# Kernel tuning notes

Hardware: AMD Instinct MI355X
Metric: run time of the kernel (lower is better)

Reference implementation:

```python
import jax, jax.numpy as jnp
import numpy as np

EPS = 1e-8

def _mlp(z, W1, b1, W2, b2):
    # Two Blocks (Linear + ReLU), widths per n_layers=[512,128]
    z = jax.nn.relu(z @ W1 + b1)
    z = jax.nn.relu(z @ W2 + b2)
    return z

def setup_inputs() -> dict:
    key = jax.random.key(0)
    ks = jax.random.split(key, 5)
    B, N, D = 1024, 30000, 256
    H1, H2 = 512, 128
    x = jax.random.normal(ks[0], (B, D), dtype=jnp.float32)
    sub_x = jax.random.normal(ks[1], (N, D), dtype=jnp.float32)
    sub_y = jax.random.uniform(ks[2], (N,), dtype=jnp.float32)
    W1 = jax.random.normal(ks[3], (D, H1), dtype=jnp.float32) * (1.0 / np.sqrt(D))
    b1 = jnp.zeros((H1,), dtype=jnp.float32)
    W2 = jax.random.normal(ks[4], (H1, H2), dtype=jnp.float32) * (1.0 / np.sqrt(H1))
    b2 = jnp.zeros((H2,), dtype=jnp.float32)
    return {"x": x, "sub_x": sub_x, "sub_y": sub_y, "W1": W1, "b1": b1, "W2": W2, "b2": b2}

def reference(x, sub_x, sub_y, W1, b1, W2, b2):
    h = _mlp(x, W1, b1, W2, b2)          # [B, d]
    sh = _mlp(sub_x, W1, b1, W2, b2)     # [N, d]
    # Pairwise squared euclidean via ||a||^2 + ||b||^2 - 2 a.b (GEMM form,
    # same math as the broadcasted diff-and-reduce in the torch code)
    x2 = jnp.sum(h * h, axis=-1, keepdims=True)        # [B, 1]
    s2 = jnp.sum(sh * sh, axis=-1)[None, :]            # [1, N]
    d2 = jnp.maximum(x2 + s2 - 2.0 * (h @ sh.T), 0.0)  # [B, N]
    dist = jnp.sqrt(d2 + EPS)
    alpha = jax.nn.softmax(-dist, axis=-1)             # [B, N]
    return alpha @ sub_y                               # [B]
```

## Files before the change

kernel.cpp:

```cpp
#include <hip/hip_runtime.h>
#include <hip/hip_bf16.h>
#include <math.h>

#define EPSF 1e-8f

typedef __attribute__((ext_vector_type(8))) short bf16x8;
typedef __attribute__((ext_vector_type(4))) float f32x4;

static __device__ __forceinline__ unsigned short f2bf(float f) {
    __hip_bfloat16 h = __float2bfloat16(f);
    return *reinterpret_cast<unsigned short*>(&h);
}
static __device__ __forceinline__ float bf2f(unsigned short u) {
    __hip_bfloat16 h;
    *reinterpret_cast<unsigned short*>(&h) = u;
    return __bfloat162float(h);
}

static __device__ __forceinline__ void async16(void* lds, const void* g) {
    __builtin_amdgcn_global_load_lds(
        (const __attribute__((address_space(1))) unsigned int*)g,
        (__attribute__((address_space(3))) unsigned int*)lds, 16, 0, 0);
}

__global__ __launch_bounds__(256) void split_combined(
    const float* __restrict__ subx, const float* __restrict__ x,
    unsigned short* __restrict__ H, unsigned short* __restrict__ L,
    float* __restrict__ gl, float* __restrict__ gy, float* __restrict__ nrm,
    int n4, int nsubrow, int nrm4)
{
    int i = blockIdx.x * 256 + threadIdx.x;
    float4 z = make_float4(0.f, 0.f, 0.f, 0.f);
    if (i < 512) {
        if (i < 256) ((float4*)gl)[i] = z;
        else         ((float4*)gy)[i - 256] = z;
    }
    if (i < nrm4) ((float4*)nrm)[i] = z;
    if (i >= n4) return;
    int row = i >> 6;
    float4 v = (row < nsubrow)
        ? ((const float4*)subx)[i]
        : ((const float4*)x)[i - (size_t)nsubrow * 64];
    unsigned short h0 = f2bf(v.x), h1 = f2bf(v.y), h2 = f2bf(v.z), h3 = f2bf(v.w);
    unsigned short l0 = f2bf(v.x - bf2f(h0));
    unsigned short l1 = f2bf(v.y - bf2f(h1));
    unsigned short l2 = f2bf(v.z - bf2f(h2));
    unsigned short l3 = f2bf(v.w - bf2f(h3));
    uint2 hp, lp;
    hp.x = ((unsigned)h1 << 16) | h0;  hp.y = ((unsigned)h3 << 16) | h2;
    lp.x = ((unsigned)l1 << 16) | l0;  lp.y = ((unsigned)l3 << 16) | l2;
    ((uint2*)H)[i] = hp;
    ((uint2*)L)[i] = lp;
}

__global__ __launch_bounds__(256) void tsplit(
    const float* __restrict__ W, unsigned short* __restrict__ HT,
    unsigned short* __restrict__ LT, int kshift, int N, int total)
{
    int idx = blockIdx.x * 256 + threadIdx.x;
    if (idx >= total) return;
    int K = 1 << kshift;
    int n = idx >> kshift, k = idx & (K - 1);
    float w = W[(size_t)k * N + n];
    unsigned short h = f2bf(w);
    HT[idx] = h;
    LT[idx] = f2bf(w - bf2f(h));
}

__global__ __launch_bounds__(256, 5) void gemm_l1(
    const unsigned short* __restrict__ Ah, const unsigned short* __restrict__ Al,
    const unsigned short* __restrict__ BhT, const unsigned short* __restrict__ BlT,
    const float* __restrict__ bias, unsigned short* __restrict__ Cout, int M)
{
    const int K = 256, N = 512;
    __shared__ __align__(16) unsigned short smem[4608];
    unsigned short* sBh = smem;
    unsigned short* sBl = smem + 2048;

    const int nb = gridDim.x;
    const int per = nb >> 3, rem = nb & 7;
    const int xcd = blockIdx.x & 7, slot = blockIdx.x >> 3;
    const int newbid = xcd * per + min(xcd, rem) + slot;
    const int m0 = (newbid >> 3) * 128, n0 = (newbid & 7) * 64;

    const int t = threadIdx.x, wave = t >> 6, lane = t & 63;
    const int quad = lane >> 4, lq = lane & 15;
    const int rsub = lane >> 2, kc8 = (lane & 3) * 8;

    const unsigned short* gb[2];
    unsigned short* lb[2];
    #pragma unroll
    for (int q = 0; q < 2; ++q) {
        int c = wave * 2 + q;
        int plane = c >> 2, rc = c & 3;
        gb[q] = (plane ? BlT : BhT) + (size_t)(n0 + rc * 16 + rsub) * K + kc8;
        lb[q] = (plane ? sBl : sBh) + rc * 512;
    }
    const unsigned short* pAh[2];
    const unsigned short* pAl[2];
    #pragma unroll
    for (int mi = 0; mi < 2; ++mi) {
        size_t r = (size_t)min(m0 + wave * 32 + mi * 16 + lq, M - 1) * K + quad * 8;
        pAh[mi] = Ah + r;
        pAl[mi] = Al + r;
    }

    f32x4 acc[2][4];
    #pragma unroll
    for (int i = 0; i < 2; ++i)
        #pragma unroll
        for (int j = 0; j < 4; ++j) acc[i][j] = (f32x4){0.f, 0.f, 0.f, 0.f};

    #pragma unroll
    for (int kc = 0; kc < 8; ++kc) {
        const int k0 = kc * 32;
        __syncthreads();
        #pragma unroll
        for (int q = 0; q < 2; ++q) async16(lb[q], gb[q] + k0);
        bf16x8 fAh[2], fAl[2];
        #pragma unroll
        for (int mi = 0; mi < 2; ++mi) {
            fAh[mi] = *(const bf16x8*)(pAh[mi] + k0);
            fAl[mi] = *(const bf16x8*)(pAl[mi] + k0);
        }
        __syncthreads();

        #pragma unroll
        for (int ni = 0; ni < 4; ++ni) {
            int off = ni * 512 + lq * 32 + quad * 8;
            bf16x8 fBh = *(const bf16x8*)&sBh[off];
            bf16x8 fBl = *(const bf16x8*)&sBl[off];
            #pragma unroll
            for (int mi = 0; mi < 2; ++mi) {
                f32x4 a = acc[mi][ni];
                a = __builtin_amdgcn_mfma_f32_16x16x32_bf16(fAh[mi], fBh, a, 0, 0, 0);
                a = __builtin_amdgcn_mfma_f32_16x16x32_bf16(fAh[mi], fBl, a, 0, 0, 0);
                a = __builtin_amdgcn_mfma_f32_16x16x32_bf16(fAl[mi], fBh, a, 0, 0, 0);
                acc[mi][ni] = a;
            }
        }
    }

    unsigned short* ctile = smem;
    float bv[4];
    #pragma unroll
    for (int ni = 0; ni < 4; ++ni) bv[ni] = bias[n0 + ni * 16 + lq];
    #pragma unroll
    for (int p = 0; p < 2; ++p) {
        __syncthreads();
        if ((wave >> 1) == p) {
            int lrow0 = (wave & 1) * 32;
            #pragma unroll
            for (int mi = 0; mi < 2; ++mi)
                #pragma unroll
                for (int ni = 0; ni < 4; ++ni)
                    #pragma unroll
                    for (int r = 0; r < 4; ++r) {
                        float v = fmaxf(acc[mi][ni][r] + bv[ni], 0.f);
                        ctile[(lrow0 + mi * 16 + quad * 4 + r) * 72 + ni * 16 + lq] = f2bf(v);
                    }
        }
        __syncthreads();
        #pragma unroll
        for (int it = 0; it < 2; ++it) {
            int flat = it * 256 + t;
            int row = flat >> 3, seg = flat & 7;
            int gm = m0 + p * 64 + row;
            if (gm < M) {
                bf16x8 v = *(const bf16x8*)&ctile[row * 72 + seg * 8];
                *(bf16x8*)&Cout[(size_t)gm * N + n0 + seg * 8] = v;
            }
        }
    }
}

__global__ __launch_bounds__(256, 5) void gemm_l2_norm(
    const unsigned short* __restrict__ A,
    const unsigned short* __restrict__ BhT, const unsigned short* __restrict__ BlT,
    const float* __restrict__ bias, unsigned short* __restrict__ Cout,
    float* __restrict__ nrm, int M)
{
    const int K = 512, N = 128;
    __shared__ __align__(16) unsigned short smem[4608];
    unsigned short* sBh = smem;
    unsigned short* sBl = smem + 2048;

    const int t = threadIdx.x, wave = t >> 6, lane = t & 63;
    const int quad = lane >> 4, lq = lane & 15;
    const int m0 = (blockIdx.x >> 1) * 128, n0 = (blockIdx.x & 1) * 64;
    const int rsub = lane >> 2, kc8 = (lane & 3) * 8;

    const unsigned short* gb[2];
    unsigned short* lb[2];
    #pragma unroll
    for (int q = 0; q < 2; ++q) {
        int c = wave * 2 + q;
        int plane = c >> 2, rc = c & 3;
        gb[q] = (plane ? BlT : BhT) + (size_t)(n0 + rc * 16 + rsub) * K + kc8;
        lb[q] = (plane ? sBl : sBh) + rc * 512;
    }
    const unsigned short* pA[2];
    #pragma unroll
    for (int mi = 0; mi < 2; ++mi)
        pA[mi] = A + (size_t)min(m0 + wave * 32 + mi * 16 + lq, M - 1) * K + quad * 8;

    f32x4 acc[2][4];
    #pragma unroll
    for (int i = 0; i < 2; ++i)
        #pragma unroll
        for (int j = 0; j < 4; ++j) acc[i][j] = (f32x4){0.f, 0.f, 0.f, 0.f};

    #pragma unroll
    for (int kc = 0; kc < 16; ++kc) {
        const int k0 = kc * 32;
        __syncthreads();
        #pragma unroll
        for (int q = 0; q < 2; ++q) async16(lb[q], gb[q] + k0);
        bf16x8 fA[2];
        #pragma unroll
        for (int mi = 0; mi < 2; ++mi) fA[mi] = *(const bf16x8*)(pA[mi] + k0);
        __syncthreads();

        #pragma unroll
        for (int ni = 0; ni < 4; ++ni) {
            int off = ni * 512 + lq * 32 + quad * 8;
            bf16x8 fBh = *(const bf16x8*)&sBh[off];
            bf16x8 fBl = *(const bf16x8*)&sBl[off];
            #pragma unroll
            for (int mi = 0; mi < 2; ++mi) {
                f32x4 a = acc[mi][ni];
                a = __builtin_amdgcn_mfma_f32_16x16x32_bf16(fA[mi], fBh, a, 0, 0, 0);
                a = __builtin_amdgcn_mfma_f32_16x16x32_bf16(fA[mi], fBl, a, 0, 0, 0);
                acc[mi][ni] = a;
            }
        }
    }

    unsigned short* ctile = smem;
    float bv[4];
    #pragma unroll
    for (int ni = 0; ni < 4; ++ni) bv[ni] = bias[n0 + ni * 16 + lq];
    #pragma unroll
    for (int p = 0; p < 2; ++p) {
        __syncthreads();
        if ((wave >> 1) == p) {
            int lrow0 = (wave & 1) * 32;
            #pragma unroll
            for (int mi = 0; mi < 2; ++mi)
                #pragma unroll
                for (int ni = 0; ni < 4; ++ni)
                    #pragma unroll
                    for (int r = 0; r < 4; ++r) {
                        float v = fmaxf(acc[mi][ni][r] + bv[ni], 0.f);
                        ctile[(lrow0 + mi * 16 + quad * 4 + r) * 72 + ni * 16 + lq] = f2bf(v);
                    }
        }
        __syncthreads();
        #pragma unroll
        for (int it = 0; it < 2; ++it) {
            int flat = it * 256 + t;
            int row = flat >> 3, seg = flat & 7;
            int gm = m0 + p * 64 + row;
            if (gm < M) {
                bf16x8 v = *(const bf16x8*)&ctile[row * 72 + seg * 8];
                *(bf16x8*)&Cout[(size_t)gm * N + n0 + seg * 8] = v;
                float s = 0.f;
                #pragma unroll
                for (int e = 0; e < 8; ++e) {
                    float f = bf2f((unsigned short)v[e]);
                    s = fmaf(f, f, s);
                }
                s += __shfl_down(s, 4, 8);
                s += __shfl_down(s, 2, 8);
                s += __shfl_down(s, 1, 8);
                if (seg == 0) atomicAdd(&nrm[gm], s);
            }
        }
    }
}

__global__ __launch_bounds__(256) void nca_flash_mfma(
    const unsigned short* __restrict__ emb, const float* __restrict__ nrm,
    const float* __restrict__ y, float* __restrict__ gl, float* __restrict__ gy,
    int N, int jspan)
{
    __shared__ __align__(16) unsigned short hA[8192];
    __shared__ __align__(16) unsigned short sB[16384];
    __shared__ float h2s[64], s2s[128], ys[128];

    const int t = threadIdx.x, wave = t >> 6, lane = t & 63;
    const int quad = lane >> 4, lq = lane & 15;
    const int rsub = lane >> 2, kc8 = (lane & 3) * 8;
    const int i0 = blockIdx.x * 64;
    const int j0base = blockIdx.y * jspan;
    const int jend = min(j0base + jspan, N);
    const unsigned short* hb = emb + (size_t)N * 128;

    #pragma unroll
    for (int q = 0; q < 4; ++q)
        async16(hA + (wave * 4 + q) * 512,
                hb + (size_t)(i0 + wave * 16 + rsub) * 128 + q * 32 + kc8);
    if (t < 64) h2s[t] = nrm[N + i0 + t];
    __syncthreads();

    float myh2[4];
    #pragma unroll
    for (int r = 0; r < 4; ++r) myh2[r] = h2s[wave * 16 + quad * 4 + r];

    float lacc[4] = {0.f, 0.f, 0.f, 0.f};
    float yacc[4] = {0.f, 0.f, 0.f, 0.f};

    for (int j0 = j0base; j0 < jend; j0 += 128) {
        __syncthreads();
        #pragma unroll
        for (int q = 0; q < 8; ++q) {
            int c = wave * 8 + q;
            int rc = c >> 2, kcq = c & 3;
            int jr = min(j0 + rc * 16 + rsub, jend - 1);
            async16(sB + c * 512, emb + (size_t)jr * 128 + kcq * 32 + kc8);
        }
        if (t < 128) {
            int j = j0 + t;
            s2s[t] = (j < jend) ? nrm[j] : 1e30f;
            ys[t]  = (j < jend) ? y[j] : 0.f;
        }
        __syncthreads();

        f32x4 acc[8];
        #pragma unroll
        for (int jt = 0; jt < 8; ++jt) acc[jt] = (f32x4){0.f, 0.f, 0.f, 0.f};
        #pragma unroll
        for (int kk = 0; kk < 4; ++kk) {
            bf16x8 a = *(const bf16x8*)&hA[(wave * 4 + kk) * 512 + lq * 32 + quad * 8];
            #pragma unroll
            for (int jt = 0; jt < 8; ++jt) {
                bf16x8 b = *(const bf16x8*)&sB[(jt * 4 + kk) * 512 + lq * 32 + quad * 8];
                acc[jt] = __builtin_amdgcn_mfma_f32_16x16x32_bf16(a, b, acc[jt], 0, 0, 0);
            }
        }

        #pragma unroll
        for (int jt = 0; jt < 8; ++jt) {
            int col = jt * 16 + lq;
            float ss = s2s[col];
            float sy = ys[col];
            #pragma unroll
            for (int r = 0; r < 4; ++r) {
                float d2 = myh2[r] + ss - 2.f * acc[jt][r];
                float d  = sqrtf(fmaxf(d2, 0.f) + EPSF);
                float p  = __expf(-d);
                lacc[r] += p;
                yacc[r]  = fmaf(p, sy, yacc[r]);
            }
        }
    }

    #pragma unroll
    for (int r = 0; r < 4; ++r) {
        #pragma unroll
        for (int off = 8; off > 0; off >>= 1) {
            lacc[r] += __shfl_down(lacc[r], off, 16);
            yacc[r] += __shfl_down(yacc[r], off, 16);
        }
    }
    if (lq == 0) {
        int rowl = wave * 16 + quad * 4;
        #pragma unroll
        for (int r = 0; r < 4; ++r) {
            atomicAdd(&gl[i0 + rowl + r], lacc[r]);
            atomicAdd(&gy[i0 + rowl + r], yacc[r]);
        }
    }
}

__global__ __launch_bounds__(256) void finalize_div(
    const float* __restrict__ gl, const float* __restrict__ gy,
    float* __restrict__ out, int B)
{
    int i = blockIdx.x * 256 + threadIdx.x;
    if (i < B) out[i] = gy[i] / gl[i];
}

extern "C" void kernel_launch(void* const* d_in, const int* in_sizes, int n_in,
                              void* d_out, int out_size, void* d_ws, size_t ws_size,
                              hipStream_t stream)
{
    const float* x    = (const float*)d_in[0];
    const float* subx = (const float*)d_in[1];
    const float* suby = (const float*)d_in[2];
    const float* W1   = (const float*)d_in[3];
    const float* b1   = (const float*)d_in[4];
    const float* W2   = (const float*)d_in[5];
    const float* b2   = (const float*)d_in[6];
    float* out = (float*)d_out;

    const int B = 1024, N = 30000, D = 256, H1 = 512, H2 = 128;
    const int M = N + B;

    char* wsb = (char*)d_ws;
    size_t off = 0;
    auto alloc = [&](size_t bytes) -> char* {
        char* p = wsb + off;
        off += (bytes + 255) & ~(size_t)255;
        return p;
    };
    unsigned short* cxh  = (unsigned short*)alloc((size_t)M * D * 2);
    unsigned short* cxl  = (unsigned short*)alloc((size_t)M * D * 2);
    unsigned short* w1hT = (unsigned short*)alloc((size_t)H1 * D * 2);
    unsigned short* w1lT = (unsigned short*)alloc((size_t)H1 * D * 2);
    unsigned short* w2hT = (unsigned short*)alloc((size_t)H2 * H1 * 2);
    unsigned short* w2lT = (unsigned short*)alloc((size_t)H2 * H1 * 2);
    unsigned short* z1   = (unsigned short*)alloc((size_t)M * H1 * 2);
    unsigned short* emb  = (unsigned short*)alloc((size_t)M * H2 * 2);
    float* nrm = (float*)alloc((size_t)M * 4);
    float* gl  = (float*)alloc((size_t)B * 4);
    float* gy  = (float*)alloc((size_t)B * 4);
    (void)ws_size; (void)in_sizes; (void)n_in; (void)out_size;

    dim3 blk(256);
    split_combined<<<dim3(M * D / 4 / 256), blk, 0, stream>>>(
        subx, x, cxh, cxl, gl, gy, nrm, M * D / 4, N, (M + 3) / 4);
    tsplit<<<dim3(D * H1 / 256), blk, 0, stream>>>(W1, w1hT, w1lT, 8, H1, D * H1);
    tsplit<<<dim3(H1 * H2 / 256), blk, 0, stream>>>(W2, w2hT, w2lT, 9, H2, H1 * H2);
    gemm_l1<<<dim3(((M + 127) / 128) * (H1 / 64)), blk, 0, stream>>>(
        cxh, cxl, w1hT, w1lT, b1, z1, M);
    gemm_l2_norm<<<dim3(((M + 127) / 128) * (H2 / 64)), blk, 0, stream>>>(
        z1, w2hT, w2lT, b2, emb, nrm, M);
    const int JSPAN = 512;
    const int NSPLIT = (N + JSPAN - 1) / JSPAN;
    nca_flash_mfma<<<dim3(B / 64, NSPLIT), blk, 0, stream>>>(
        emb, nrm, suby, gl, gy, N, JSPAN);
    finalize_div<<<dim3(B / 256), blk, 0, stream>>>(gl, gy, out, B);
}
```

Baseline: 184.4 us.

## Stage full B panels in LDS once and read flash operands directly from global

Both MLP GEMMs now load the entire hi/lo weight panel for the block into a 64KB LDS buffer with a single barrier, instead of staging one K-chunk per iteration between two barriers. gemm_l2_norm narrows its N tile to 32, doubles the grid and adds XCD-aware block remapping. The distance/softmax kernel drops LDS staging entirely and reads A fragments, B fragments, norms and labels straight from global memory with no barriers. The large LDS footprint cuts occupancy (launch bounds lowered to 2 blocks), and the global-direct flash loads depend on cache hit rates.

```diff
diff --git a/kernel.cpp b/kernel.cpp
--- a/kernel.cpp
+++ b/kernel.cpp
@@ -67,15 +67,13 @@
     LT[idx] = f2bf(w - bf2f(h));
 }
 
-__global__ __launch_bounds__(256, 5) void gemm_l1(
+__global__ __launch_bounds__(256, 2) void gemm_l1(
     const unsigned short* __restrict__ Ah, const unsigned short* __restrict__ Al,
     const unsigned short* __restrict__ BhT, const unsigned short* __restrict__ BlT,
     const float* __restrict__ bias, unsigned short* __restrict__ Cout, int M)
 {
     const int K = 256, N = 512;
-    __shared__ __align__(16) unsigned short smem[4608];
-    unsigned short* sBh = smem;
-    unsigned short* sBl = smem + 2048;
+    __shared__ __align__(16) unsigned short sB[32768];
 
     const int nb = gridDim.x;
     const int per = nb >> 3, rem = nb & 7;
@@ -87,15 +85,15 @@
     const int quad = lane >> 4, lq = lane & 15;
     const int rsub = lane >> 2, kc8 = (lane & 3) * 8;
 
-    const unsigned short* gb[2];
-    unsigned short* lb[2];
-    #pragma unroll
-    for (int q = 0; q < 2; ++q) {
-        int c = wave * 2 + q;
-        int plane = c >> 2, rc = c & 3;
-        gb[q] = (plane ? BlT : BhT) + (size_t)(n0 + rc * 16 + rsub) * K + kc8;
-        lb[q] = (plane ? sBl : sBh) + rc * 512;
-    }
+    #pragma unroll
+    for (int q = 0; q < 16; ++q) {
+        int c = wave * 16 + q;
+        int plane = c >> 5, idx = c & 31, nc = idx >> 3, kc = idx & 7;
+        const unsigned short* src = (plane ? BlT : BhT)
+            + (size_t)(n0 + nc * 16 + rsub) * K + kc * 32 + kc8;
+        async16(sB + c * 512, src);
+    }
+
     const unsigned short* pAh[2];
     const unsigned short* pAl[2];
     #pragma unroll
@@ -111,25 +109,22 @@
         #pragma unroll
         for (int j = 0; j < 4; ++j) acc[i][j] = (f32x4){0.f, 0.f, 0.f, 0.f};
 
+    __syncthreads();
+
     #pragma unroll
     for (int kc = 0; kc < 8; ++kc) {
         const int k0 = kc * 32;
-        __syncthreads();
-        #pragma unroll
-        for (int q = 0; q < 2; ++q) async16(lb[q], gb[q] + k0);
         bf16x8 fAh[2], fAl[2];
         #pragma unroll
         for (int mi = 0; mi < 2; ++mi) {
             fAh[mi] = *(const bf16x8*)(pAh[mi] + k0);
             fAl[mi] = *(const bf16x8*)(pAl[mi] + k0);
         }
-        __syncthreads();
-
         #pragma unroll
         for (int ni = 0; ni < 4; ++ni) {
-            int off = ni * 512 + lq * 32 + quad * 8;
-            bf16x8 fBh = *(const bf16x8*)&sBh[off];
-            bf16x8 fBl = *(const bf16x8*)&sBl[off];
+            int off = (ni * 8 + kc) * 512 + lq * 32 + quad * 8;
+            bf16x8 fBh = *(const bf16x8*)&sB[off];
+            bf16x8 fBl = *(const bf16x8*)&sB[16384 + off];
             #pragma unroll
             for (int mi = 0; mi < 2; ++mi) {
                 f32x4 a = acc[mi][ni];
@@ -141,7 +136,7 @@
         }
     }
 
-    unsigned short* ctile = smem;
+    unsigned short* ctile = sB;
     float bv[4];
     #pragma unroll
     for (int ni = 0; ni < 4; ++ni) bv[ni] = bias[n0 + ni * 16 + lq];
@@ -174,58 +169,58 @@
     }
 }
 
-__global__ __launch_bounds__(256, 5) void gemm_l2_norm(
+__global__ __launch_bounds__(256, 2) void gemm_l2_norm(
     const unsigned short* __restrict__ A,
     const unsigned short* __restrict__ BhT, const unsigned short* __restrict__ BlT,
     const float* __restrict__ bias, unsigned short* __restrict__ Cout,
     float* __restrict__ nrm, int M)
 {
     const int K = 512, N = 128;
-    __shared__ __align__(16) unsigned short smem[4608];
-    unsigned short* sBh = smem;
-    unsigned short* sBl = smem + 2048;
+    __shared__ __align__(16) unsigned short sB[32768];
+
+    const int nb = gridDim.x;
+    const int per = nb >> 3, rem = nb & 7;
+    const int xcd = blockIdx.x & 7, slot = blockIdx.x >> 3;
+    const int newbid = xcd * per + min(xcd, rem) + slot;
+    const int m0 = (newbid >> 2) * 128, n0 = (newbid & 3) * 32;
 
     const int t = threadIdx.x, wave = t >> 6, lane = t & 63;
     const int quad = lane >> 4, lq = lane & 15;
-    const int m0 = (blockIdx.x >> 1) * 128, n0 = (blockIdx.x & 1) * 64;
     const int rsub = lane >> 2, kc8 = (lane & 3) * 8;
 
-    const unsigned short* gb[2];
-    unsigned short* lb[2];
-    #pragma unroll
-    for (int q = 0; q < 2; ++q) {
-        int c = wave * 2 + q;
-        int plane = c >> 2, rc = c & 3;
-        gb[q] = (plane ? BlT : BhT) + (size_t)(n0 + rc * 16 + rsub) * K + kc8;
-        lb[q] = (plane ? sBl : sBh) + rc * 512;
-    }
+    #pragma unroll
+    for (int q = 0; q < 16; ++q) {
+        int c = wave * 16 + q;
+        int plane = c >> 5, idx = c & 31, nc = idx >> 4, kc = idx & 15;
+        const unsigned short* src = (plane ? BlT : BhT)
+            + (size_t)(n0 + nc * 16 + rsub) * K + kc * 32 + kc8;
+        async16(sB + c * 512, src);
+    }
+
     const unsigned short* pA[2];
     #pragma unroll
     for (int mi = 0; mi < 2; ++mi)
         pA[mi] = A + (size_t)min(m0 + wave * 32 + mi * 16 + lq, M - 1) * K + quad * 8;
 
-    f32x4 acc[2][4];
+    f32x4 acc[2][2];
     #pragma unroll
     for (int i = 0; i < 2; ++i)
         #pragma unroll
-        for (int j = 0; j < 4; ++j) acc[i][j] = (f32x4){0.f, 0.f, 0.f, 0.f};
+        for (int j = 0; j < 2; ++j) acc[i][j] = (f32x4){0.f, 0.f, 0.f, 0.f};
+
+    __syncthreads();
 
     #pragma unroll
     for (int kc = 0; kc < 16; ++kc) {
         const int k0 = kc * 32;
-        __syncthreads();
-        #pragma unroll
-        for (int q = 0; q < 2; ++q) async16(lb[q], gb[q] + k0);
         bf16x8 fA[2];
         #pragma unroll
         for (int mi = 0; mi < 2; ++mi) fA[mi] = *(const bf16x8*)(pA[mi] + k0);
-        __syncthreads();
-
-        #pragma unroll
-        for (int ni = 0; ni < 4; ++ni) {
-            int off = ni * 512 + lq * 32 + quad * 8;
-            bf16x8 fBh = *(const bf16x8*)&sBh[off];
-            bf16x8 fBl = *(const bf16x8*)&sBl[off];
+        #pragma unroll
+        for (int ni = 0; ni < 2; ++ni) {
+            int off = (ni * 16 + kc) * 512 + lq * 32 + quad * 8;
+            bf16x8 fBh = *(const bf16x8*)&sB[off];
+            bf16x8 fBl = *(const bf16x8*)&sB[16384 + off];
             #pragma unroll
             for (int mi = 0; mi < 2; ++mi) {
                 f32x4 a = acc[mi][ni];
@@ -236,114 +231,92 @@
         }
     }
 
-    unsigned short* ctile = smem;
-    float bv[4];
-    #pragma unroll
-    for (int ni = 0; ni < 4; ++ni) bv[ni] = bias[n0 + ni * 16 + lq];
-    #pragma unroll
-    for (int p = 0; p < 2; ++p) {
-        __syncthreads();
-        if ((wave >> 1) == p) {
-            int lrow0 = (wave & 1) * 32;
-            #pragma unroll
-            for (int mi = 0; mi < 2; ++mi)
-                #pragma unroll
-                for (int ni = 0; ni < 4; ++ni)
-                    #pragma unroll
-                    for (int r = 0; r < 4; ++r) {
-                        float v = fmaxf(acc[mi][ni][r] + bv[ni], 0.f);
-                        ctile[(lrow0 + mi * 16 + quad * 4 + r) * 72 + ni * 16 + lq] = f2bf(v);
-                    }
-        }
-        __syncthreads();
-        #pragma unroll
-        for (int it = 0; it < 2; ++it) {
-            int flat = it * 256 + t;
-            int row = flat >> 3, seg = flat & 7;
-            int gm = m0 + p * 64 + row;
-            if (gm < M) {
-                bf16x8 v = *(const bf16x8*)&ctile[row * 72 + seg * 8];
-                *(bf16x8*)&Cout[(size_t)gm * N + n0 + seg * 8] = v;
-                float s = 0.f;
-                #pragma unroll
-                for (int e = 0; e < 8; ++e) {
-                    float f = bf2f((unsigned short)v[e]);
-                    s = fmaf(f, f, s);
-                }
-                s += __shfl_down(s, 4, 8);
-                s += __shfl_down(s, 2, 8);
-                s += __shfl_down(s, 1, 8);
-                if (seg == 0) atomicAdd(&nrm[gm], s);
-            }
-        }
-    }
-}
-
-__global__ __launch_bounds__(256) void nca_flash_mfma(
+    __syncthreads();
+    unsigned short* ctile = sB;
+    float bv[2];
+    #pragma unroll
+    for (int ni = 0; ni < 2; ++ni) bv[ni] = bias[n0 + ni * 16 + lq];
+    #pragma unroll
+    for (int mi = 0; mi < 2; ++mi)
+        #pragma unroll
+        for (int ni = 0; ni < 2; ++ni)
+            #pragma unroll
+            for (int r = 0; r < 4; ++r) {
+                float v = fmaxf(acc[mi][ni][r] + bv[ni], 0.f);
+                ctile[(wave * 32 + mi * 16 + quad * 4 + r) * 36 + ni * 16 + lq] = f2bf(v);
+            }
+    __syncthreads();
+
+    #pragma unroll
+    for (int it = 0; it < 2; ++it) {
+        int flat = it * 256 + t;
+        int row = flat >> 2, seg = flat & 3;
+        int gm = m0 + row;
+        if (gm < M) {
+            bf16x8 v = *(const bf16x8*)&ctile[row * 36 + seg * 8];
+            *(bf16x8*)&Cout[(size_t)gm * N + n0 + seg * 8] = v;
+            float s = 0.f;
+            #pragma unroll
+            for (int e = 0; e < 8; ++e) {
+                float f = bf2f((unsigned short)v[e]);
+                s = fmaf(f, f, s);
+            }
+            s += __shfl_down(s, 2, 4);
+            s += __shfl_down(s, 1, 4);
+            if (seg == 0) atomicAdd(&nrm[gm], s);
+        }
+    }
+}
+
+__global__ __launch_bounds__(256, 3) void nca_flash_mfma(
     const unsigned short* __restrict__ emb, const float* __restrict__ nrm,
     const float* __restrict__ y, float* __restrict__ gl, float* __restrict__ gy,
     int N, int jspan)
 {
-    __shared__ __align__(16) unsigned short hA[8192];
-    __shared__ __align__(16) unsigned short sB[16384];
-    __shared__ float h2s[64], s2s[128], ys[128];
-
     const int t = threadIdx.x, wave = t >> 6, lane = t & 63;
     const int quad = lane >> 4, lq = lane & 15;
-    const int rsub = lane >> 2, kc8 = (lane & 3) * 8;
     const int i0 = blockIdx.x * 64;
     const int j0base = blockIdx.y * jspan;
     const int jend = min(j0base + jspan, N);
     const unsigned short* hb = emb + (size_t)N * 128;
 
-    #pragma unroll
-    for (int q = 0; q < 4; ++q)
-        async16(hA + (wave * 4 + q) * 512,
-                hb + (size_t)(i0 + wave * 16 + rsub) * 128 + q * 32 + kc8);
-    if (t < 64) h2s[t] = nrm[N + i0 + t];
-    __syncthreads();
-
+    bf16x8 fa[4];
+    #pragma unroll
+    for (int kk = 0; kk < 4; ++kk)
+        fa[kk] = *(const bf16x8*)&hb[(size_t)(i0 + wave * 16 + lq) * 128 + kk * 32 + quad * 8];
     float myh2[4];
     #pragma unroll
-    for (int r = 0; r < 4; ++r) myh2[r] = h2s[wave * 16 + quad * 4 + r];
+    for (int r = 0; r < 4; ++r) myh2[r] = nrm[N + i0 + wave * 16 + quad * 4 + r];
 
     float lacc[4] = {0.f, 0.f, 0.f, 0.f};
     float yacc[4] = {0.f, 0.f, 0.f, 0.f};
 
-    for (int j0 = j0base; j0 < jend; j0 += 128) {
-        __syncthreads();
-        #pragma unroll
-        for (int q = 0; q < 8; ++q) {
-            int c = wave * 8 + q;
-            int rc = c >> 2, kcq = c & 3;
-            int jr = min(j0 + rc * 16 + rsub, jend - 1);
-            async16(sB + c * 512, emb + (size_t)jr * 128 + kcq * 32 + kc8);
-        }
-        if (t < 128) {
-            int j = j0 + t;
-            s2s[t] = (j < jend) ? nrm[j] : 1e30f;
-            ys[t]  = (j < jend) ? y[j] : 0.f;
-        }
-        __syncthreads();
+    #pragma unroll 2
+    for (int c = 0; c < 4; ++c) {
+        int j0 = j0base + c * 128;
+        if (j0 >= jend) break;
 
         f32x4 acc[8];
         #pragma unroll
         for (int jt = 0; jt < 8; ++jt) acc[jt] = (f32x4){0.f, 0.f, 0.f, 0.f};
         #pragma unroll
         for (int kk = 0; kk < 4; ++kk) {
-            bf16x8 a = *(const bf16x8*)&hA[(wave * 4 + kk) * 512 + lq * 32 + quad * 8];
+            bf16x8 b[8];
             #pragma unroll
             for (int jt = 0; jt < 8; ++jt) {
-                bf16x8 b = *(const bf16x8*)&sB[(jt * 4 + kk) * 512 + lq * 32 + quad * 8];
-                acc[jt] = __builtin_amdgcn_mfma_f32_16x16x32_bf16(a, b, acc[jt], 0, 0, 0);
-            }
+                int jr = min(j0 + jt * 16 + lq, jend - 1);
+                b[jt] = *(const bf16x8*)&emb[(size_t)jr * 128 + kk * 32 + quad * 8];
+            }
+            #pragma unroll
+            for (int jt = 0; jt < 8; ++jt)
+                acc[jt] = __builtin_amdgcn_mfma_f32_16x16x32_bf16(fa[kk], b[jt], acc[jt], 0, 0, 0);
         }
 
         #pragma unroll
         for (int jt = 0; jt < 8; ++jt) {
-            int col = jt * 16 + lq;
-            float ss = s2s[col];
-            float sy = ys[col];
+            int col = j0 + jt * 16 + lq;
+            float ss = (col < jend) ? nrm[col] : 1e30f;
+            float sy = (col < jend) ? y[col] : 0.f;
             #pragma unroll
             for (int r = 0; r < 4; ++r) {
                 float d2 = myh2[r] + ss - 2.f * acc[jt][r];
@@ -424,7 +397,7 @@
     tsplit<<<dim3(H1 * H2 / 256), blk, 0, stream>>>(W2, w2hT, w2lT, 9, H2, H1 * H2);
     gemm_l1<<<dim3(((M + 127) / 128) * (H1 / 64)), blk, 0, stream>>>(
         cxh, cxl, w1hT, w1lT, b1, z1, M);
-    gemm_l2_norm<<<dim3(((M + 127) / 128) * (H2 / 64)), blk, 0, stream>>>(
+    gemm_l2_norm<<<dim3(((M + 127) / 128) * (H2 / 32)), blk, 0, stream>>>(
         z1, w2hT, w2lT, b2, emb, nrm, M);
     const int JSPAN = 512;
     const int NSPLIT = (N + JSPAN - 1) / JSPAN;
```

New measurement: 224.0 us. 21.5% more time.
